# Kernel tuning notes

Hardware: AMD Instinct MI355X
Metric: run time of the kernel (lower is better)

## Reference

```python
import jax, jax.numpy as jnp
import numpy as np

B, S, H = 1, 4096, 2048
NH, NKV, HD = 16, 4, 128
EPS = 1e-5
THETA = 10000.0


def rms_norm(x, w, eps=EPS):
    var = jnp.mean(jnp.square(x), axis=-1, keepdims=True)
    return x * jax.lax.rsqrt(var + eps) * w


def rotate_half(x):
    x1, x2 = jnp.split(x, 2, axis=-1)
    return jnp.concatenate([-x2, x1], axis=-1)


def rope_cos_sin(seq_len, head_dim, dtype):
    inv_freq = 1.0 / (THETA ** (jnp.arange(0, head_dim, 2, dtype=jnp.float32) / head_dim))
    t = jnp.arange(seq_len, dtype=jnp.float32)
    freqs = jnp.outer(t, inv_freq)                      # [S, HD/2]
    emb = jnp.concatenate([freqs, freqs], axis=-1)      # [S, HD]
    return jnp.cos(emb).astype(dtype), jnp.sin(emb).astype(dtype)


def setup_inputs() -> dict:
    key = jax.random.key(0)
    ks = jax.random.split(key, 5)
    return {
        "hidden_states": jax.random.normal(ks[0], (B, S, H), jnp.float32),
        "wq": jax.random.normal(ks[1], (NH * HD, H), jnp.float32) * 0.02,
        "wk": jax.random.normal(ks[2], (NKV * HD, H), jnp.float32) * 0.02,
        "wv": jax.random.normal(ks[3], (NKV * HD, H), jnp.float32) * 0.02,
        "wo": jax.random.normal(ks[4], (H, NH * HD), jnp.float32) * 0.02,
        "q_norm_w": jnp.ones((NH * HD,), jnp.float32),
        "k_norm_w": jnp.ones((NKV * HD,), jnp.float32),
    }


def reference(hidden_states, wq, wk, wv, wo, q_norm_w, k_norm_w):
    b, s, _ = hidden_states.shape
    n_rep = NH // NKV

    # projections + QK RMSNorm (applied over the full flattened head dim, pre-split)
    q = rms_norm(hidden_states @ wq.T, q_norm_w)        # [B,S,NH*HD]
    k = rms_norm(hidden_states @ wk.T, k_norm_w)        # [B,S,NKV*HD]
    v = hidden_states @ wv.T                            # [B,S,NKV*HD]

    # split heads -> [B, heads, S, HD]
    q = q.reshape(b, s, NH, HD).transpose(0, 2, 1, 3)
    k = k.reshape(b, s, NKV, HD).transpose(0, 2, 1, 3)
    v = v.reshape(b, s, NKV, HD).transpose(0, 2, 1, 3)

    # RoPE (position_ids = arange(s))
    cos, sin = rope_cos_sin(s, HD, q.dtype)             # [S, HD]
    cos = cos[None, None]                               # [1,1,S,HD]
    sin = sin[None, None]
    q = q * cos + rotate_half(q) * sin
    k = k * cos + rotate_half(k) * sin

    # GQA attention without physical KV repeat: q -> [B, NKV, n_rep, S, HD]
    qg = q.reshape(b, NKV, n_rep, s, HD)
    scale = 1.0 / np.sqrt(HD)
    scores = jnp.einsum('bgrqd,bgkd->bgrqk', qg, k) * scale   # [B,NKV,rep,S,S]

    causal = jnp.tril(jnp.ones((s, s), bool))
    scores = jnp.where(causal, scores, jnp.finfo(scores.dtype).min)

    probs = jax.nn.softmax(scores.astype(jnp.float32), axis=-1).astype(q.dtype)
    out = jnp.einsum('bgrqk,bgkd->bgrqd', probs, v)           # [B,NKV,rep,S,HD]

    # merge heads -> [B,S,NH*HD], output projection
    out = out.reshape(b, NH, s, HD).transpose(0, 2, 1, 3).reshape(b, s, NH * HD)
    return out @ wo.T
```

## Files before the change

### kernel.cpp

```cpp
#include <hip/hip_runtime.h>
#include <math.h>

#define S_LEN 4096
#define HIDDEN 2048
#define N_HEADS 16
#define N_KV 4
#define HEAD_DIM 128
#define QDIM 2048
#define KDIM 512
#define QKVD 3072
#define QSCALE 0.1275174486f

typedef __bf16 bf16x8 __attribute__((ext_vector_type(8)));
typedef float f32x4 __attribute__((ext_vector_type(4)));
typedef float f32x16 __attribute__((ext_vector_type(16)));

__device__ __forceinline__ unsigned short f2bf(float x) {
  union { float f; unsigned u; } v; v.f = x;
  unsigned r = v.u + 0x7fffu + ((v.u >> 16) & 1u);
  return (unsigned short)(r >> 16);
}
__device__ __forceinline__ float bf2f(unsigned short u) {
  union { unsigned u; float f; } v; v.u = ((unsigned)u) << 16;
  return v.f;
}

__device__ __forceinline__ float wave_sum(float x) {
#pragma unroll
  for (int w = 32; w >= 1; w >>= 1) x += __shfl_xor(x, w);
  return x;
}

__global__ void k_cvt(const float* __restrict__ s, unsigned short* __restrict__ d, int n4) {
  int i = blockIdx.x * blockDim.x + threadIdx.x;
  if (i >= n4) return;
  float4 v = reinterpret_cast<const float4*>(s)[i];
  ushort4 o;
  o.x = f2bf(v.x); o.y = f2bf(v.y); o.z = f2bf(v.z); o.w = f2bf(v.w);
  reinterpret_cast<ushort4*>(d)[i] = o;
}

__global__ void k_rope_tab(float* __restrict__ cosT, float* __restrict__ sinT) {
  int idx = blockIdx.x * blockDim.x + threadIdx.x;
  int s = idx >> 6, d = idx & 63;
  float inv = powf(10000.0f, -(float)(2 * d) * (1.0f / 128.0f));
  float f = (float)s * inv;
  cosT[idx] = cosf(f);
  sinT[idx] = sinf(f);
}

#define GKT (HIDDEN / 64)

template <int BF16OUT>
__global__ __launch_bounds__(256, 2) void k_gemm(
    const unsigned short* __restrict__ A, const unsigned short* __restrict__ B,
    void* __restrict__ Cv, int N) {
  __shared__ char ldsb[65536];
  const int tid = threadIdx.x;
  const int w = tid >> 6, lane = tid & 63;
  const int l15 = lane & 15, g16 = lane >> 4;
  const int wm = w >> 1, wn = w & 1;
  const int brow = blockIdx.y * 128, bcol = blockIdx.x * 128;
  const char* Abp = (const char*)(A + (size_t)brow * HIDDEN);
  const char* Bbp = (const char*)(B + (size_t)bcol * HIDDEN);

#define GSTAGE(bi, kt)                                                              \
  {                                                                                 \
    _Pragma("unroll")                                                               \
    for (int j = 0; j < 4; ++j) {                                                   \
      const int slot = w * 256 + j * 64 + lane;                                     \
      const int r = slot >> 3;                                                      \
      const int cb = (slot & 7) * 16;                                               \
      const char* srcA = Abp + (size_t)r * (2 * HIDDEN) + (kt) * 128 +              \
                         (cb ^ ((r & 7) << 4));                                     \
      __builtin_amdgcn_global_load_lds(                                             \
          (const __attribute__((address_space(1))) void*)srcA,                      \
          (__attribute__((address_space(3))) void*)(ldsb + (bi)*16384 + slot * 16), \
          16, 0, 0);                                                                \
      const char* srcB = Bbp + (size_t)r * (2 * HIDDEN) + (kt) * 128 +              \
                         (cb ^ ((r & 7) << 4));                                     \
      __builtin_amdgcn_global_load_lds(                                             \
          (const __attribute__((address_space(1))) void*)srcB,                      \
          (__attribute__((address_space(3))) void*)(ldsb + 32768 + (bi)*16384 +     \
                                                    slot * 16),                     \
          16, 0, 0);                                                                \
    }                                                                               \
  }

  f32x4 acc[4][4] = {};

  GSTAGE(0, 0)
  GSTAGE(1, 1)
  asm volatile("s_waitcnt vmcnt(8)" ::: "memory");
  __builtin_amdgcn_sched_barrier(0);
  __builtin_amdgcn_s_barrier();
  __builtin_amdgcn_sched_barrier(0);

  for (int kt = 0; kt < GKT; ++kt) {
    const char* Al = ldsb + (kt & 1) * 16384;
    const char* Bl = ldsb + 32768 + (kt & 1) * 16384;
    bf16x8 a[4][2], b[4][2];
#pragma unroll
    for (int fm = 0; fm < 4; ++fm) {
      const int r = wm * 64 + fm * 16 + l15;
#pragma unroll
      for (int kh = 0; kh < 2; ++kh)
        a[fm][kh] = *reinterpret_cast<const bf16x8*>(
            Al + r * 128 + ((kh * 64 + g16 * 16) ^ ((r & 7) << 4)));
    }
#pragma unroll
    for (int fn = 0; fn < 4; ++fn) {
      const int r = wn * 64 + fn * 16 + l15;
#pragma unroll
      for (int kh = 0; kh < 2; ++kh)
        b[fn][kh] = *reinterpret_cast<const bf16x8*>(
            Bl + r * 128 + ((kh * 64 + g16 * 16) ^ ((r & 7) << 4)));
    }
    asm volatile("s_waitcnt lgkmcnt(0)" ::: "memory");
    __builtin_amdgcn_sched_barrier(0);
    __builtin_amdgcn_s_barrier();
    __builtin_amdgcn_sched_barrier(0);
    if (kt + 2 < GKT) GSTAGE(kt & 1, kt + 2)
    __builtin_amdgcn_s_setprio(1);
#pragma unroll
    for (int kh = 0; kh < 2; ++kh)
#pragma unroll
      for (int fm = 0; fm < 4; ++fm)
#pragma unroll
        for (int fn = 0; fn < 4; ++fn)
          acc[fm][fn] =
              __builtin_amdgcn_mfma_f32_16x16x32_bf16(a[fm][kh], b[fn][kh], acc[fm][fn], 0, 0, 0);
    __builtin_amdgcn_s_setprio(0);
    if (kt + 1 < GKT) {
      if (kt + 2 < GKT) {
        asm volatile("s_waitcnt vmcnt(8)" ::: "memory");
      } else {
        asm volatile("s_waitcnt vmcnt(0)" ::: "memory");
      }
      __builtin_amdgcn_sched_barrier(0);
      __builtin_amdgcn_s_barrier();
      __builtin_amdgcn_sched_barrier(0);
    }
  }

  const int crow = brow + wm * 64 + g16 * 4;
  const int ccol = bcol + wn * 64 + l15;
#pragma unroll
  for (int fm = 0; fm < 4; ++fm)
#pragma unroll
    for (int fn = 0; fn < 4; ++fn)
#pragma unroll
      for (int i = 0; i < 4; ++i) {
        const size_t off = (size_t)(crow + fm * 16 + i) * N + ccol + fn * 16;
        if (BF16OUT)
          ((unsigned short*)Cv)[off] = f2bf(acc[fm][fn][i]);
        else
          ((float*)Cv)[off] = acc[fm][fn][i];
      }
#undef GSTAGE
}

__global__ __launch_bounds__(256) void k_norm_rope(
    const unsigned short* __restrict__ QKV, const float* __restrict__ qw,
    const float* __restrict__ kw, const float* __restrict__ cosT,
    const float* __restrict__ sinT, unsigned short* __restrict__ Q,
    unsigned short* __restrict__ Kd, unsigned short* __restrict__ Vt) {
  const int s = blockIdx.x;
  const int tid = threadIdx.x;
  const int lane = tid & 63, wave = tid >> 6;
  const unsigned short* row = QKV + (size_t)s * QKVD;
  __shared__ float sm[QDIM];
  __shared__ float red[4];

  float qv[8];
  {
    uint4 r = *reinterpret_cast<const uint4*>(row + tid * 8);
    unsigned u[4] = {r.x, r.y, r.z, r.w};
#pragma unroll
    for (int j = 0; j < 4; ++j) {
      qv[2 * j] = bf2f((unsigned short)(u[j] & 0xffff));
      qv[2 * j + 1] = bf2f((unsigned short)(u[j] >> 16));
    }
  }
  float ss = 0;
#pragma unroll
  for (int j = 0; j < 8; ++j) ss += qv[j] * qv[j];
  ss = wave_sum(ss);
  if (lane == 0) red[wave] = ss;
  __syncthreads();
  float tot = red[0] + red[1] + red[2] + red[3];
  float qs = rsqrtf(tot * (1.0f / QDIM) + 1e-5f) * QSCALE;
#pragma unroll
  for (int j = 0; j < 8; ++j) sm[tid * 8 + j] = qv[j] * qs * qw[tid * 8 + j];
  __syncthreads();
  {
    const int d0 = tid * 8;
    const int h = d0 >> 7;
    const int dh = d0 & 127;
    const int dc = dh & 63;
    const bool lo = dh < 64;
    const float sgn = lo ? -1.0f : 1.0f;
    const int po = lo ? 64 : -64;
    union { unsigned short b[8]; uint4 u; } pk;
#pragma unroll
    for (int j = 0; j < 8; ++j) {
      float c = cosT[s * 64 + dc + j];
      float sn = sinT[s * 64 + dc + j];
      float o = sm[d0 + j] * c + sgn * sm[d0 + po + j] * sn;
      pk.b[j] = f2bf(o);
    }
    *reinterpret_cast<uint4*>(Q + ((size_t)h * S_LEN + s) * HEAD_DIM + dh) = pk.u;
  }
  __syncthreads();

  float kx, ky;
  {
    unsigned kr = *reinterpret_cast<const unsigned*>(row + QDIM + tid * 2);
    kx = bf2f((unsigned short)(kr & 0xffff));
    ky = bf2f((unsigned short)(kr >> 16));
  }
  ss = kx * kx + ky * ky;
  ss = wave_sum(ss);
  if (lane == 0) red[wave] = ss;
  __syncthreads();
  tot = red[0] + red[1] + red[2] + red[3];
  float ks = rsqrtf(tot * (1.0f / KDIM) + 1e-5f);
  sm[tid * 2] = kx * ks * kw[tid * 2];
  sm[tid * 2 + 1] = ky * ks * kw[tid * 2 + 1];
  __syncthreads();
  {
    const int d0 = tid * 2;
    const int g = d0 >> 7;
    const int dh = d0 & 127;
    const int dc = dh & 63;
    const bool lo = dh < 64;
    const float sgn = lo ? -1.0f : 1.0f;
    const int po = lo ? 64 : -64;
    union { unsigned short b[2]; unsigned u; } pk;
#pragma unroll
    for (int j = 0; j < 2; ++j) {
      float c = cosT[s * 64 + dc + j];
      float sn = sinT[s * 64 + dc + j];
      float o = sm[d0 + j] * c + sgn * sm[d0 + po + j] * sn;
      pk.b[j] = f2bf(o);
    }
    *reinterpret_cast<unsigned*>(Kd + ((size_t)g * S_LEN + s) * HEAD_DIM + dh) = pk.u;
  }

  {
    unsigned vr = *reinterpret_cast<const unsigned*>(row + QDIM + KDIM + tid * 2);
    int dv = tid * 2;
    int g = dv >> 7, d = dv & 127;
    Vt[(size_t)(g * HEAD_DIM + d) * S_LEN + s] = (unsigned short)(vr & 0xffff);
    Vt[(size_t)(g * HEAD_DIM + d + 1) * S_LEN + s] = (unsigned short)(vr >> 16);
  }
}

__global__ __launch_bounds__(256, 3) void k_attn(
    const unsigned short* __restrict__ Q, const unsigned short* __restrict__ K,
    const unsigned short* __restrict__ Vt,
    unsigned short* __restrict__ Op0, unsigned short* __restrict__ Op1,
    float* __restrict__ Mp, float* __restrict__ Lp) {
  const int bid = blockIdx.x;
  const int qt = 127 - (bid >> 3);
  const int sub = bid & 7;
  const int g = sub >> 1, half = sub & 1;
  const int NT = qt + 1, ntlo = (NT + 1) >> 1;
  const int t0 = half ? ntlo : 0, t1 = half ? NT : ntlo;

  const int tid = threadIdx.x;
  const int w = tid >> 6, lane = tid & 63;
  const int l31 = lane & 31, g2 = lane >> 5;
  const int h = g * 4 + w;
  const int qpos = qt * 32;

  unsigned short* __restrict__ Op = half ? Op1 : Op0;
  float* __restrict__ Mh = Mp + half * (16 * 4096);
  float* __restrict__ Lh = Lp + half * (16 * 4096);

  if (t0 >= t1) {
    if (g2 == 0) {
      Mh[h * 4096 + qpos + l31] = -1e30f;
      Lh[h * 4096 + qpos + l31] = 0.f;
    }
    return;
  }

  __shared__ char lds[2][16384];

  const char* Kgb = (const char*)(K + (size_t)g * S_LEN * HEAD_DIM);
  const char* Vgb = (const char*)(Vt + (size_t)g * HEAD_DIM * S_LEN);

  const bool isK = (w < 2);
  const int wj = isK ? w : (w - 2);

#define STAGE(BUFP, KV0)                                                                  \
  {                                                                                       \
    char* dstb = (BUFP);                                                                  \
    _Pragma("unroll")                                                                     \
    for (int j = 0; j < 4; ++j) {                                                         \
      if (isK) {                                                                          \
        const int r = (wj * 4 + j) * 4 + (lane >> 4);                                     \
        const char* src = Kgb + (size_t)((KV0) + r) * 256 +                               \
                          (((lane & 15) * 16) ^ ((r & 15) << 4));                         \
        __builtin_amdgcn_global_load_lds(                                                 \
            (const __attribute__((address_space(1))) void*)src,                           \
            (__attribute__((address_space(3))) void*)(dstb + (wj * 4 + j) * 1024),        \
            16, 0, 0);                                                                    \
      } else {                                                                            \
        const int r = (wj * 4 + j) * 8 + (lane >> 3);                                     \
        const int cu = ((lane & 7) * 16) ^ ((r & 7) << 4);                                \
        const int dd = 2 * r + (cu >> 6);                                                 \
        const char* src = Vgb + (size_t)dd * 8192 + (size_t)(KV0) * 2 + (cu & 63);        \
        __builtin_amdgcn_global_load_lds(                                                 \
            (const __attribute__((address_space(1))) void*)src,                           \
            (__attribute__((address_space(3))) void*)(dstb + 8192 + (wj * 4 + j) * 1024), \
            16, 0, 0);                                                                    \
      }                                                                                   \
    }                                                                                     \
  }

  STAGE(lds[0], t0 * 32)

  bf16x8 qf[8];
#pragma unroll
  for (int dc2 = 0; dc2 < 8; ++dc2)
    qf[dc2] = *reinterpret_cast<const bf16x8*>(
        Q + ((size_t)h * S_LEN + qpos + l31) * HEAD_DIM + dc2 * 16 + g2 * 8);

  f32x16 o[4] = {};
  float m = -1e30f, l = 0.f;

  for (int t = t0; t < t1; ++t) {
    char* buf = lds[(t - t0) & 1];
    __syncthreads();
    if (t + 1 < t1) STAGE(lds[(t - t0 + 1) & 1], (t + 1) * 32)
    const char* Kl = buf;
    const char* Vl = buf + 8192;
    const int kv0 = t * 32;

    f32x16 sc = {};
    __builtin_amdgcn_s_setprio(1);
#pragma unroll
    for (int dc2 = 0; dc2 < 8; ++dc2) {
      bf16x8 kf = *reinterpret_cast<const bf16x8*>(
          Kl + l31 * 256 + ((dc2 * 32 + g2 * 16) ^ ((l31 & 15) << 4)));
      sc = __builtin_amdgcn_mfma_f32_32x32x16_bf16(kf, qf[dc2], sc, 0, 0, 0);
    }
    __builtin_amdgcn_s_setprio(0);
    if (t == qt) {
#pragma unroll
      for (int reg = 0; reg < 16; ++reg) {
        int kv = kv0 + (reg & 3) + 8 * (reg >> 2) + 4 * g2;
        if (kv > qpos + l31) sc[reg] = -1e30f;
      }
    }
    float pm = sc[0];
#pragma unroll
    for (int i = 1; i < 16; ++i) pm = fmaxf(pm, sc[i]);
    pm = fmaxf(pm, __shfl_xor(pm, 32));
    if (!__all(pm <= m + 8.f)) {
      float mn = fmaxf(m, pm);
      float fac = __builtin_amdgcn_exp2f(m - mn);
#pragma unroll
      for (int dc = 0; dc < 4; ++dc) o[dc] *= fac;
      l *= fac;
      m = mn;
    }
    union { __bf16 b[16]; unsigned u[8]; } P;
    float rs = 0.f;
#pragma unroll
    for (int i = 0; i < 16; ++i) {
      float p = __builtin_amdgcn_exp2f(sc[i] - m);
      rs += p;
      P.b[i] = (__bf16)p;
    }
    rs += __shfl_xor(rs, 32);
    l += rs;
    uint4 pf[2];
#pragma unroll
    for (int c16 = 0; c16 < 2; ++c16) {
      unsigned A0 = P.u[c16 * 4], A1 = P.u[c16 * 4 + 1];
      unsigned A2 = P.u[c16 * 4 + 2], A3 = P.u[c16 * 4 + 3];
      unsigned A0x = __shfl_xor(A0, 32), A1x = __shfl_xor(A1, 32);
      unsigned A2x = __shfl_xor(A2, 32), A3x = __shfl_xor(A3, 32);
      pf[c16].x = g2 ? A2x : A0;
      pf[c16].y = g2 ? A3x : A1;
      pf[c16].z = g2 ? A2 : A0x;
      pf[c16].w = g2 ? A3 : A1x;
    }
    __builtin_amdgcn_s_setprio(1);
#pragma unroll
    for (int c16 = 0; c16 < 2; ++c16) {
      union { uint4 u; bf16x8 v; } cv;
      cv.u = pf[c16];
#pragma unroll
      for (int dc = 0; dc < 4; ++dc) {
        const int r = dc * 16 + (l31 >> 1);
        const int cu = (l31 & 1) * 64 + c16 * 32 + g2 * 16;
        bf16x8 vf = *reinterpret_cast<const bf16x8*>(Vl + r * 128 + (cu ^ ((r & 7) << 4)));
        o[dc] = __builtin_amdgcn_mfma_f32_32x32x16_bf16(vf, cv.v, o[dc], 0, 0, 0);
      }
    }
    __builtin_amdgcn_s_setprio(0);
  }

  if (g2 == 0) {
    Mh[h * 4096 + qpos + l31] = m;
    Lh[h * 4096 + qpos + l31] = l;
  }
#pragma unroll
  for (int dc = 0; dc < 4; ++dc)
#pragma unroll
    for (int reg = 0; reg < 16; ++reg) {
      int d = dc * 32 + (reg & 3) + 8 * (reg >> 2) + 4 * g2;
      Op[(((size_t)(h * 128 + d)) << 12) + qpos + l31] = f2bf(o[dc][reg]);
    }
#undef STAGE
}

__global__ __launch_bounds__(256) void k_combine(
    const unsigned short* __restrict__ Op0, const unsigned short* __restrict__ Op1,
    const float* __restrict__ Mp, const float* __restrict__ Lp,
    unsigned short* __restrict__ AO) {
  const int idx = blockIdx.x * 256 + threadIdx.x;
  const int h = idx >> 12, q = idx & 4095;
  const float m0 = Mp[h * 4096 + q], m1 = Mp[16 * 4096 + h * 4096 + q];
  const float l0 = Lp[h * 4096 + q], l1 = Lp[16 * 4096 + h * 4096 + q];
  const float mm = fmaxf(m0, m1);
  const float w0 = __builtin_amdgcn_exp2f(m0 - mm);
  const float w1 = __builtin_amdgcn_exp2f(m1 - mm);
  const float denom = w0 * l0 + w1 * l1;
  const float c0 = w0 / denom, c1 = w1 / denom;
  const bool has1 = (l1 > 0.f);
  const size_t bq = ((size_t)h * 128) << 12;
#pragma unroll
  for (int halfd = 0; halfd < 2; ++halfd) {
    float acc[64];
#pragma unroll
    for (int i = 0; i < 64; ++i) {
      const size_t off = bq + (((size_t)(halfd * 64 + i)) << 12) + q;
      float v = c0 * bf2f(Op0[off]);
      if (has1) v += c1 * bf2f(Op1[off]);
      acc[i] = v;
    }
#pragma unroll
    for (int dc = 0; dc < 8; ++dc) {
      union { unsigned short s[8]; uint4 u; } pk;
#pragma unroll
      for (int j = 0; j < 8; ++j) pk.s[j] = f2bf(acc[dc * 8 + j]);
      *reinterpret_cast<uint4*>(AO + (size_t)q * QDIM + h * 128 + halfd * 64 + dc * 8) = pk.u;
    }
  }
}

extern "C" void kernel_launch(void* const* d_in, const int* in_sizes, int n_in,
                              void* d_out, int out_size, void* d_ws, size_t ws_size,
                              hipStream_t stream) {
  const float* hs = (const float*)d_in[0];
  const float* wq = (const float*)d_in[1];
  const float* wk = (const float*)d_in[2];
  const float* wv = (const float*)d_in[3];
  const float* wo = (const float*)d_in[4];
  const float* qnw = (const float*)d_in[5];
  const float* knw = (const float*)d_in[6];
  float* out = (float*)d_out;

  char* base = (char*)d_ws;
  unsigned short* Xb = (unsigned short*)base;
  unsigned short* Qb = Xb;
  unsigned short* Wqkv = (unsigned short*)(base + 16777216);
  unsigned short* Kb = Wqkv;
  unsigned short* Vtb = (unsigned short*)(base + 20971520);
  float* Mp = (float*)(base + 25165824);
  float* Lp = (float*)(base + 25690112);
  unsigned short* Wob = (unsigned short*)(base + 29360128);
  unsigned short* QKVb = (unsigned short*)(base + 37748736);
  unsigned short* AOb = QKVb;
  unsigned short* Op0 = (unsigned short*)(base + 54525952);
  unsigned short* Op1 = (unsigned short*)(base + 71303168);
  float* cosT = (float*)(base + 88080384);
  float* sinT = (float*)(base + 89128960);

  int n;
  n = S_LEN * HIDDEN / 4; k_cvt<<<(n + 255) / 256, 256, 0, stream>>>(hs, Xb, n);
  n = QDIM * HIDDEN / 4;  k_cvt<<<(n + 255) / 256, 256, 0, stream>>>(wq, Wqkv, n);
  n = KDIM * HIDDEN / 4;  k_cvt<<<(n + 255) / 256, 256, 0, stream>>>(wk, Wqkv + (size_t)QDIM * HIDDEN, n);
  n = KDIM * HIDDEN / 4;  k_cvt<<<(n + 255) / 256, 256, 0, stream>>>(wv, Wqkv + (size_t)(QDIM + KDIM) * HIDDEN, n);
  n = HIDDEN * QDIM / 4;  k_cvt<<<(n + 255) / 256, 256, 0, stream>>>(wo, Wob, n);
  k_rope_tab<<<(S_LEN * 64) / 256, 256, 0, stream>>>(cosT, sinT);

  k_gemm<1><<<dim3(QKVD / 128, S_LEN / 128), 256, 0, stream>>>(Xb, Wqkv, (void*)QKVb, QKVD);
  k_norm_rope<<<S_LEN, 256, 0, stream>>>(QKVb, qnw, knw, cosT, sinT, Qb, Kb, Vtb);
  k_attn<<<1024, 256, 0, stream>>>(Qb, Kb, Vtb, Op0, Op1, Mp, Lp);
  k_combine<<<256, 256, 0, stream>>>(Op0, Op1, Mp, Lp, AOb);
  k_gemm<0><<<dim3(QDIM / 128, S_LEN / 128), 256, 0, stream>>>(AOb, Wob, (void*)out, QDIM);
}
```

Baseline: 314.1 us.

## Fuse prep kernels, swizzle GEMM workgroups across XCDs, restructure GEMM barriers

Replaces the six conversion and RoPE-table launches with one grid-stride prep kernel, which removes per-launch overhead and tail effects. Remaps GEMM workgroup IDs in an 8-way XCD-aware swizzle so neighbouring tiles share L2. Reorders the GEMM main loop so the next-stage prefetch is issued after the MFMAs and drops the lgkmcnt wait, the setprio calls and some sched barriers. The prefetch now overwrites the buffer only after a barrier that follows compute, but dropping the explicit LDS wait before the MFMAs relies on the compiler to insert it.

Result: no change. 308.4 us (median of 2 runs) (-1.8%).

```diff
diff --git a/kernel.cpp b/kernel.cpp
--- a/kernel.cpp
+++ b/kernel.cpp
@@ -31,22 +31,45 @@
   return x;
 }
 
-__global__ void k_cvt(const float* __restrict__ s, unsigned short* __restrict__ d, int n4) {
-  int i = blockIdx.x * blockDim.x + threadIdx.x;
-  if (i >= n4) return;
+__device__ __forceinline__ void cvt4(const float* __restrict__ s,
+                                     unsigned short* __restrict__ d, int i) {
   float4 v = reinterpret_cast<const float4*>(s)[i];
   ushort4 o;
   o.x = f2bf(v.x); o.y = f2bf(v.y); o.z = f2bf(v.z); o.w = f2bf(v.w);
   reinterpret_cast<ushort4*>(d)[i] = o;
 }
 
-__global__ void k_rope_tab(float* __restrict__ cosT, float* __restrict__ sinT) {
-  int idx = blockIdx.x * blockDim.x + threadIdx.x;
-  int s = idx >> 6, d = idx & 63;
-  float inv = powf(10000.0f, -(float)(2 * d) * (1.0f / 128.0f));
-  float f = (float)s * inv;
-  cosT[idx] = cosf(f);
-  sinT[idx] = sinf(f);
+__global__ __launch_bounds__(256) void k_prep(
+    const float* __restrict__ hs, const float* __restrict__ wq, const float* __restrict__ wk,
+    const float* __restrict__ wv, const float* __restrict__ wo,
+    unsigned short* __restrict__ Xb, unsigned short* __restrict__ Wqkv,
+    unsigned short* __restrict__ Wob, float* __restrict__ cosT, float* __restrict__ sinT) {
+  const int NHS = (S_LEN * HIDDEN) / 4;
+  const int NWQ = (QDIM * HIDDEN) / 4;
+  const int NWK = (KDIM * HIDDEN) / 4;
+  const int NWV = (KDIM * HIDDEN) / 4;
+  const int NWO = (HIDDEN * QDIM) / 4;
+  const int NRT = S_LEN * 64;
+  const int TOT = NHS + NWQ + NWK + NWV + NWO + NRT;
+  const int stride = gridDim.x * 256;
+  for (int i = blockIdx.x * 256 + threadIdx.x; i < TOT; i += stride) {
+    int j = i;
+    if (j < NHS) { cvt4(hs, Xb, j); continue; }
+    j -= NHS;
+    if (j < NWQ) { cvt4(wq, Wqkv, j); continue; }
+    j -= NWQ;
+    if (j < NWK) { cvt4(wk, Wqkv + (size_t)QDIM * HIDDEN, j); continue; }
+    j -= NWK;
+    if (j < NWV) { cvt4(wv, Wqkv + (size_t)(QDIM + KDIM) * HIDDEN, j); continue; }
+    j -= NWV;
+    if (j < NWO) { cvt4(wo, Wob, j); continue; }
+    j -= NWO;
+    int s = j >> 6, d = j & 63;
+    float inv = powf(10000.0f, -(float)(2 * d) * (1.0f / 128.0f));
+    float f = (float)s * inv;
+    cosT[j] = cosf(f);
+    sinT[j] = sinf(f);
+  }
 }
 
 #define GKT (HIDDEN / 64)
@@ -60,7 +83,12 @@
   const int w = tid >> 6, lane = tid & 63;
   const int l15 = lane & 15, g16 = lane >> 4;
   const int wm = w >> 1, wn = w & 1;
-  const int brow = blockIdx.y * 128, bcol = blockIdx.x * 128;
+  const unsigned nwg = gridDim.x * gridDim.y;
+  const unsigned wg = blockIdx.y * gridDim.x + blockIdx.x;
+  const unsigned cpx = nwg >> 3;
+  const unsigned swz = (wg & 7) * cpx + (wg >> 3);
+  const int bx = swz % gridDim.x, by = swz / gridDim.x;
+  const int brow = by * 128, bcol = bx * 128;
   const char* Abp = (const char*)(A + (size_t)brow * HIDDEN);
   const char* Bbp = (const char*)(B + (size_t)bcol * HIDDEN);
 
@@ -92,9 +120,7 @@
   GSTAGE(0, 0)
   GSTAGE(1, 1)
   asm volatile("s_waitcnt vmcnt(8)" ::: "memory");
-  __builtin_amdgcn_sched_barrier(0);
   __builtin_amdgcn_s_barrier();
-  __builtin_amdgcn_sched_barrier(0);
 
   for (int kt = 0; kt < GKT; ++kt) {
     const char* Al = ldsb + (kt & 1) * 16384;
@@ -116,12 +142,6 @@
         b[fn][kh] = *reinterpret_cast<const bf16x8*>(
             Bl + r * 128 + ((kh * 64 + g16 * 16) ^ ((r & 7) << 4)));
     }
-    asm volatile("s_waitcnt lgkmcnt(0)" ::: "memory");
-    __builtin_amdgcn_sched_barrier(0);
-    __builtin_amdgcn_s_barrier();
-    __builtin_amdgcn_sched_barrier(0);
-    if (kt + 2 < GKT) GSTAGE(kt & 1, kt + 2)
-    __builtin_amdgcn_s_setprio(1);
 #pragma unroll
     for (int kh = 0; kh < 2; ++kh)
 #pragma unroll
@@ -130,16 +150,16 @@
         for (int fn = 0; fn < 4; ++fn)
           acc[fm][fn] =
               __builtin_amdgcn_mfma_f32_16x16x32_bf16(a[fm][kh], b[fn][kh], acc[fm][fn], 0, 0, 0);
-    __builtin_amdgcn_s_setprio(0);
+    __builtin_amdgcn_sched_barrier(0);
+    __builtin_amdgcn_s_barrier();
+    if (kt + 2 < GKT) GSTAGE(kt & 1, kt + 2)
     if (kt + 1 < GKT) {
       if (kt + 2 < GKT) {
         asm volatile("s_waitcnt vmcnt(8)" ::: "memory");
       } else {
         asm volatile("s_waitcnt vmcnt(0)" ::: "memory");
       }
-      __builtin_amdgcn_sched_barrier(0);
       __builtin_amdgcn_s_barrier();
-      __builtin_amdgcn_sched_barrier(0);
     }
   }
 
@@ -482,14 +502,7 @@
   float* cosT = (float*)(base + 88080384);
   float* sinT = (float*)(base + 89128960);
 
-  int n;
-  n = S_LEN * HIDDEN / 4; k_cvt<<<(n + 255) / 256, 256, 0, stream>>>(hs, Xb, n);
-  n = QDIM * HIDDEN / 4;  k_cvt<<<(n + 255) / 256, 256, 0, stream>>>(wq, Wqkv, n);
-  n = KDIM * HIDDEN / 4;  k_cvt<<<(n + 255) / 256, 256, 0, stream>>>(wk, Wqkv + (size_t)QDIM * HIDDEN, n);
-  n = KDIM * HIDDEN / 4;  k_cvt<<<(n + 255) / 256, 256, 0, stream>>>(wv, Wqkv + (size_t)(QDIM + KDIM) * HIDDEN, n);
-  n = HIDDEN * QDIM / 4;  k_cvt<<<(n + 255) / 256, 256, 0, stream>>>(wo, Wob, n);
-  k_rope_tab<<<(S_LEN * 64) / 256, 256, 0, stream>>>(cosT, sinT);
-
+  k_prep<<<2048, 256, 0, stream>>>(hs, wq, wk, wv, wo, Xb, Wqkv, Wob, cosT, sinT);
   k_gemm<1><<<dim3(QKVD / 128, S_LEN / 128), 256, 0, stream>>>(Xb, Wqkv, (void*)QKVb, QKVD);
   k_norm_rope<<<S_LEN, 256, 0, stream>>>(QKVb, qnw, knw, cosT, sinT, Qb, Kb, Vtb);
   k_attn<<<1024, 256, 0, stream>>>(Qb, Kb, Vtb, Op0, Op1, Mp, Lp);
```
